# Kernel optimization log

Measured on AMD Instinct MI355X. Metric: run time of the kernel, lower is better.

Reference implementation:

```python
import jax, jax.numpy as jnp
import numpy as np

EARLY_IT = 32                      # prefix K-columns used for the statistical test
TEST_STAT_BOUND = -2.053748910631823  # scipy.stats.norm.ppf(0.02)
EPS = 1e-12
STATS_W = 1.0                      # scalar stats affine (stats_affine_mode='scalar')
STATS_B = 0.0


def setup_inputs() -> dict:
    key = jax.random.key(0)
    k1, k2, k3 = jax.random.split(key, 3)
    M, K, N = 4096, 4096, 16384    # tokens, in_features, out_features (OPT-6.7B fc1)
    x = jax.random.normal(k1, (M, K), dtype=jnp.float32)
    weight = jax.random.normal(k2, (N, K), dtype=jnp.float32) * 0.02
    bias = jax.random.normal(k3, (N,), dtype=jnp.float32) * 0.02
    return {"x": x, "weight": weight, "bias": bias}


def reference(x, weight, bias):
    # x: [M, K], weight: [N, K], bias: [N]
    E = EARLY_IT
    inv_n = jnp.float32(1.0 / E)

    xe = x[:, :E]                                  # [M, E]
    we = weight[:, :E]                             # [N, E]
    # Partial matmul over the first E reduction columns + elementwise-squared matmul
    y1 = jnp.einsum('mk,nk->mn', xe, we)           # [M, N]
    cum_sq = jnp.einsum('mk,nk->mn', xe * xe, we * we)  # [M, N]

    # Statistical early-termination test (z-test-like)
    cur_mean = y1 * inv_n * STATS_W + STATS_B
    cur_var = (cum_sq * inv_n - cur_mean * cur_mean) * (STATS_W * STATS_W)
    denom = jnp.sqrt(jnp.maximum(cur_var * inv_n, EPS))
    test_stats = cur_mean / denom
    passed = test_stats < TEST_STAT_BOUND          # [M, N] bool: True -> skip, output 0

    # Tail GEMM over remaining K-E columns
    y_tail = jnp.einsum('mk,nk->mn', x[:, E:], weight[:, E:])
    y = y1 + y_tail + bias[None, :]
    return jnp.where(passed, jnp.float32(0.0), y)
```

## Files before the change

### kernel.cpp

```cpp
#include <hip/hip_runtime.h>
#include <cstdint>
#include <cmath>

#define MDIM 4096
#define KDIM 4096
#define NDIM 16384
#define TEST_BOUND -2.053748910631823

typedef unsigned short u16;
typedef __attribute__((ext_vector_type(8))) short short8;
typedef __attribute__((ext_vector_type(4))) float floatx4;

__device__ __forceinline__ u16 f2bf(float f) {
  union { float f; uint32_t u; } c; c.f = f;
  uint32_t r = c.u + 0x7fffu + ((c.u >> 16) & 1u);
  return (u16)(r >> 16);
}

__global__ __launch_bounds__(256) void cvt_kernel(const float4* __restrict__ in,
                                                  ushort4* __restrict__ out, int n4) {
  int stride = gridDim.x * 256;
  for (int i = blockIdx.x * 256 + threadIdx.x; i < n4; i += stride) {
    float4 v = in[i];
    ushort4 o;
    o.x = f2bf(v.x); o.y = f2bf(v.y); o.z = f2bf(v.z); o.w = f2bf(v.w);
    out[i] = o;
  }
}

__global__ __launch_bounds__(256) void stats_kernel(const float* __restrict__ x,
                                                    const float* __restrict__ w,
                                                    unsigned char* __restrict__ mask) {
  __shared__ float Xs[64][33];
  __shared__ float Ws[64][33];
  const int bn = blockIdx.x;
  const int bm = blockIdx.y;
  const int t = threadIdx.x;
  for (int e = t; e < 64 * 32; e += 256) {
    int r = e >> 5, c = e & 31;
    Xs[r][c] = x[(size_t)(bm * 64 + r) * KDIM + c];
    Ws[r][c] = w[(size_t)(bn * 64 + r) * KDIM + c];
  }
  __syncthreads();
  const int tn = (t & 15) * 4;
  const int tm = (t >> 4) * 4;
  float y1[4][4] = {}, q[4][4] = {};
  for (int k = 0; k < 32; ++k) {
    float xv[4], wv[4], xx[4], ww[4];
#pragma unroll
    for (int i = 0; i < 4; ++i) { xv[i] = Xs[tm + i][k]; xx[i] = __fmul_rn(xv[i], xv[i]); }
#pragma unroll
    for (int j = 0; j < 4; ++j) { wv[j] = Ws[tn + j][k]; ww[j] = __fmul_rn(wv[j], wv[j]); }
#pragma unroll
    for (int i = 0; i < 4; ++i)
#pragma unroll
      for (int j = 0; j < 4; ++j) {
        y1[i][j] = __fadd_rn(y1[i][j], __fmul_rn(xv[i], wv[j]));
        q[i][j]  = __fadd_rn(q[i][j],  __fmul_rn(xx[i], ww[j]));
      }
  }
#pragma unroll
  for (int i = 0; i < 4; ++i)
#pragma unroll
    for (int j = 0; j < 4; ++j) {
      float mean = __fmul_rn(y1[i][j], 0.03125f);
      float var  = __fsub_rn(__fmul_rn(q[i][j], 0.03125f), __fmul_rn(mean, mean));
      float varn = __fmul_rn(var, 0.03125f);
      float den  = __fsqrt_rn(fmaxf(varn, 1e-12f));
      float ts   = __fdiv_rn(mean, den);
      bool passed = ts < (float)TEST_BOUND;
      mask[(size_t)(bm * 64 + tm + i) * NDIM + (bn * 64 + tn + j)] = passed ? 1u : 0u;
    }
}

#define BM 256
#define BN 256
#define BK 64

typedef const __attribute__((address_space(1))) uint32_t* as1_u32p;
typedef __attribute__((address_space(3))) uint32_t* as3_u32p;

__device__ __forceinline__ void async_ld16(const void* g, void* l) {
  __builtin_amdgcn_global_load_lds((as1_u32p)g, (as3_u32p)l, 16, 0, 0);
}

__device__ __forceinline__ void stage_half(const u16* __restrict__ src, size_t grow0,
                                           int k0, u16* lds, int tid) {
  const int r = tid >> 3;
  const int c = (((tid & 7) ^ (r & 7)) << 3);
  const u16* g0 = src + (grow0 + (size_t)r) * KDIM + (size_t)(k0 + c);
  u16* l0 = lds + (size_t)(tid & ~63) * 8;
  async_ld16(g0, l0);
  async_ld16(g0 + (size_t)64 * KDIM, l0 + 4096);
}

__global__ __launch_bounds__(512, 2) void gemm_kernel(const u16* __restrict__ A,
                                                      const u16* __restrict__ B,
                                                      const float* __restrict__ bias,
                                                      const unsigned char* __restrict__ mask,
                                                      float* __restrict__ C) {
  __shared__ __align__(16) u16 As[2][BM * BK];
  __shared__ __align__(16) u16 Bs[2][BN * BK];

  const int bid = blockIdx.x;
  const int swz = (bid & 7) * ((MDIM / BM) * (NDIM / BN) / 8) + (bid >> 3);
  const int bm = swz & 15;
  const int bn = swz >> 4;

  const int tid = threadIdx.x;
  const int w = tid >> 6, l = tid & 63;
  const int lm = l & 15, quad = l >> 4;
  const int wm_i = w >> 2;
  const int wn_i = w & 3;
  const int sw8 = (lm & 7) << 3;
  const int c0 = (quad * 8) ^ sw8;
  const int c1 = (32 + quad * 8) ^ sw8;

  const size_t abase = (size_t)bm * BM;
  const size_t bbase = (size_t)bn * BN;

  floatx4 acc[8][4];
#pragma unroll
  for (int i = 0; i < 8; ++i)
#pragma unroll
    for (int j = 0; j < 4; ++j) acc[i][j] = (floatx4){0.f, 0.f, 0.f, 0.f};

  stage_half(A, abase,       0,  &As[0][0],    tid);
  stage_half(B, bbase,       0,  &Bs[0][0],    tid);
  stage_half(B, bbase + 128, 0,  &Bs[0][8192], tid);
  stage_half(A, abase + 128, 0,  &As[0][8192], tid);
  asm volatile("s_waitcnt vmcnt(4)" ::: "memory");
  stage_half(A, abase,       BK, &As[1][0],    tid);
  stage_half(B, bbase,       BK, &Bs[1][0],    tid);
  stage_half(B, bbase + 128, BK, &Bs[1][8192], tid);
  asm volatile("s_waitcnt vmcnt(6)" ::: "memory");
  __builtin_amdgcn_s_barrier();

  short8 a[4][2], b[4][2];

  for (int kt = 0; kt < KDIM / BK; ++kt) {
    u16* Ab = &As[kt & 1][0];
    u16* Bb = &Bs[kt & 1][0];
    const int kn1 = (kt + 1 <= 63 ? kt + 1 : 63) * BK;
    const int kn2 = (kt + 2 <= 63 ? kt + 2 : 63) * BK;

#pragma unroll
    for (int i4 = 0; i4 < 4; ++i4) {
      const int row = wm_i * 16 + i4 * 32 + lm;
      a[i4][0] = *(const short8*)&Ab[row * 64 + c0];
      a[i4][1] = *(const short8*)&Ab[row * 64 + c1];
    }
#pragma unroll
    for (int j = 0; j < 2; ++j) {
      const int row = wn_i * 16 + j * 64 + lm;
      b[j][0] = *(const short8*)&Bb[row * 64 + c0];
      b[j][1] = *(const short8*)&Bb[row * 64 + c1];
    }
    stage_half(A, abase + 128, kn1, &As[(kt + 1) & 1][8192], tid);
    __builtin_amdgcn_s_barrier();
    asm volatile("s_waitcnt lgkmcnt(0)" ::: "memory");
    __builtin_amdgcn_sched_barrier(0);
    __builtin_amdgcn_s_setprio(1);
#pragma unroll
    for (int i4 = 0; i4 < 4; ++i4)
#pragma unroll
      for (int j = 0; j < 2; ++j) {
        acc[i4][j] = __builtin_amdgcn_mfma_f32_16x16x32_bf16(a[i4][0], b[j][0], acc[i4][j], 0, 0, 0);
        acc[i4][j] = __builtin_amdgcn_mfma_f32_16x16x32_bf16(a[i4][1], b[j][1], acc[i4][j], 0, 0, 0);
      }
    __builtin_amdgcn_s_setprio(0);
    __builtin_amdgcn_s_barrier();

#pragma unroll
    for (int j = 2; j < 4; ++j) {
      const int row = wn_i * 16 + j * 64 + lm;
      b[j][0] = *(const short8*)&Bb[row * 64 + c0];
      b[j][1] = *(const short8*)&Bb[row * 64 + c1];
    }
    stage_half(A, abase, kn2, &As[kt & 1][0], tid);
    __builtin_amdgcn_s_barrier();
    asm volatile("s_waitcnt lgkmcnt(0)" ::: "memory");
    __builtin_amdgcn_sched_barrier(0);
    __builtin_amdgcn_s_setprio(1);
#pragma unroll
    for (int i4 = 0; i4 < 4; ++i4)
#pragma unroll
      for (int j = 2; j < 4; ++j) {
        acc[i4][j] = __builtin_amdgcn_mfma_f32_16x16x32_bf16(a[i4][0], b[j][0], acc[i4][j], 0, 0, 0);
        acc[i4][j] = __builtin_amdgcn_mfma_f32_16x16x32_bf16(a[i4][1], b[j][1], acc[i4][j], 0, 0, 0);
      }
    __builtin_amdgcn_s_setprio(0);
    __builtin_amdgcn_s_barrier();

#pragma unroll
    for (int i4 = 0; i4 < 4; ++i4) {
      const int row = wm_i * 16 + (4 + i4) * 32 + lm;
      a[i4][0] = *(const short8*)&Ab[row * 64 + c0];
      a[i4][1] = *(const short8*)&Ab[row * 64 + c1];
    }
    stage_half(B, bbase, kn2, &Bs[kt & 1][0], tid);
    __builtin_amdgcn_s_barrier();
    asm volatile("s_waitcnt lgkmcnt(0)" ::: "memory");
    __builtin_amdgcn_sched_barrier(0);
    __builtin_amdgcn_s_setprio(1);
#pragma unroll
    for (int i4 = 0; i4 < 4; ++i4)
#pragma unroll
      for (int j = 0; j < 2; ++j) {
        acc[4 + i4][j] = __builtin_amdgcn_mfma_f32_16x16x32_bf16(a[i4][0], b[j][0], acc[4 + i4][j], 0, 0, 0);
        acc[4 + i4][j] = __builtin_amdgcn_mfma_f32_16x16x32_bf16(a[i4][1], b[j][1], acc[4 + i4][j], 0, 0, 0);
      }
    __builtin_amdgcn_s_setprio(0);
    __builtin_amdgcn_s_barrier();

    stage_half(B, bbase + 128, kn2, &Bs[kt & 1][8192], tid);
    __builtin_amdgcn_s_barrier();
    __builtin_amdgcn_s_setprio(1);
#pragma unroll
    for (int i4 = 0; i4 < 4; ++i4)
#pragma unroll
      for (int j = 2; j < 4; ++j) {
        acc[4 + i4][j] = __builtin_amdgcn_mfma_f32_16x16x32_bf16(a[i4][0], b[j][0], acc[4 + i4][j], 0, 0, 0);
        acc[4 + i4][j] = __builtin_amdgcn_mfma_f32_16x16x32_bf16(a[i4][1], b[j][1], acc[4 + i4][j], 0, 0, 0);
      }
    __builtin_amdgcn_s_setprio(0);
    asm volatile("s_waitcnt vmcnt(6)" ::: "memory");
    __builtin_amdgcn_s_barrier();
  }

  float bv[4];
#pragma unroll
  for (int j = 0; j < 4; ++j) bv[j] = bias[bbase + wn_i * 16 + j * 64 + lm];
#pragma unroll
  for (int i = 0; i < 8; ++i) {
    const int mrow = wm_i * 16 + i * 32 + quad * 4;
#pragma unroll
    for (int r = 0; r < 4; ++r) {
      const size_t gm = abase + (size_t)(mrow + r);
      const size_t rowoff = gm * NDIM + bbase;
#pragma unroll
      for (int j = 0; j < 4; ++j) {
        const size_t off = rowoff + (size_t)(wn_i * 16 + j * 64 + lm);
        float y = acc[i][j][r] + bv[j];
        C[off] = mask[off] ? 0.0f : y;
      }
    }
  }
}

extern "C" void kernel_launch(void* const* d_in, const int* in_sizes, int n_in,
                              void* d_out, int out_size, void* d_ws, size_t ws_size,
                              hipStream_t stream) {
  const float* x = (const float*)d_in[0];
  const float* w = (const float*)d_in[1];
  const float* bias = (const float*)d_in[2];
  float* out = (float*)d_out;

  u16* xbf = (u16*)d_ws;
  u16* wbf = xbf + (size_t)MDIM * KDIM;
  unsigned char* mask = (unsigned char*)(wbf + (size_t)NDIM * KDIM);

  cvt_kernel<<<2048, 256, 0, stream>>>((const float4*)x, (ushort4*)xbf, MDIM * KDIM / 4);
  cvt_kernel<<<8192, 256, 0, stream>>>((const float4*)w, (ushort4*)wbf, NDIM * KDIM / 4);
  stats_kernel<<<dim3(NDIM / 64, MDIM / 64), 256, 0, stream>>>(x, w, mask);
  gemm_kernel<<<(MDIM / BM) * (NDIM / BN), 512, 0, stream>>>(xbf, wbf, bias, mask, out);
}
```

Measured before the change: 1.195 ms.

## Switch GEMM inner loop to 32x32x16 bf16 MFMA tiles

Replaces the 16x16x32 MFMA tiling with 32x32x16 MFMA instructions. Each wave now holds 4x2 floatx16 accumulators instead of 8x4 floatx4. Fewer, larger MFMAs need less LDS fragment traffic per FLOP, and a partial lgkmcnt wait lets the first MFMAs start before all fragment loads land. The prefetch k-index clamps at the last tile were removed, so the final iterations may read past K into adjacent rows of the workspace. The epilogue store indexing was rewritten for the 32x32 output layout.

```diff
diff --git a/kernel.cpp b/kernel.cpp
--- a/kernel.cpp
+++ b/kernel.cpp
@@ -9,7 +9,7 @@
 
 typedef unsigned short u16;
 typedef __attribute__((ext_vector_type(8))) short short8;
-typedef __attribute__((ext_vector_type(4))) float floatx4;
+typedef __attribute__((ext_vector_type(16))) float floatx16;
 
 __device__ __forceinline__ u16 f2bf(float f) {
   union { float f; uint32_t u; } c; c.f = f;
@@ -103,27 +103,34 @@
   __shared__ __align__(16) u16 Bs[2][BN * BK];
 
   const int bid = blockIdx.x;
-  const int swz = (bid & 7) * ((MDIM / BM) * (NDIM / BN) / 8) + (bid >> 3);
+  const int swz = (bid & 7) * 128 + (bid >> 3);
   const int bm = swz & 15;
   const int bn = swz >> 4;
 
   const int tid = threadIdx.x;
   const int w = tid >> 6, l = tid & 63;
-  const int lm = l & 15, quad = l >> 4;
+  const int ln = l & 31;
+  const int kh = (l >> 5) << 3;
   const int wm_i = w >> 2;
   const int wn_i = w & 3;
-  const int sw8 = (lm & 7) << 3;
-  const int c0 = (quad * 8) ^ sw8;
-  const int c1 = (32 + quad * 8) ^ sw8;
+  const int swx = (ln & 7) << 3;
+
+  int ck[4];
+#pragma unroll
+  for (int ks = 0; ks < 4; ++ks) ck[ks] = (ks * 16 + kh) ^ swx;
+  const int arow = (wm_i * 32 + ln) * 64;
+  const int brow = (wn_i * 32 + ln) * 64;
 
   const size_t abase = (size_t)bm * BM;
   const size_t bbase = (size_t)bn * BN;
 
-  floatx4 acc[8][4];
-#pragma unroll
-  for (int i = 0; i < 8; ++i)
-#pragma unroll
-    for (int j = 0; j < 4; ++j) acc[i][j] = (floatx4){0.f, 0.f, 0.f, 0.f};
+  floatx16 acc[4][2];
+#pragma unroll
+  for (int i = 0; i < 4; ++i)
+#pragma unroll
+    for (int j = 0; j < 2; ++j)
+#pragma unroll
+      for (int r = 0; r < 16; ++r) acc[i][j][r] = 0.f;
 
   stage_half(A, abase,       0,  &As[0][0],    tid);
   stage_half(B, bbase,       0,  &Bs[0][0],    tid);
@@ -136,111 +143,98 @@
   asm volatile("s_waitcnt vmcnt(6)" ::: "memory");
   __builtin_amdgcn_s_barrier();
 
-  short8 a[4][2], b[4][2];
+  short8 a[2][4], b[2][4];
 
   for (int kt = 0; kt < KDIM / BK; ++kt) {
     u16* Ab = &As[kt & 1][0];
     u16* Bb = &Bs[kt & 1][0];
-    const int kn1 = (kt + 1 <= 63 ? kt + 1 : 63) * BK;
-    const int kn2 = (kt + 2 <= 63 ? kt + 2 : 63) * BK;
-
-#pragma unroll
-    for (int i4 = 0; i4 < 4; ++i4) {
-      const int row = wm_i * 16 + i4 * 32 + lm;
-      a[i4][0] = *(const short8*)&Ab[row * 64 + c0];
-      a[i4][1] = *(const short8*)&Ab[row * 64 + c1];
-    }
+    const int kn1 = (kt + 1) * BK;
+    const int kn2 = (kt + 2) * BK;
+
+#pragma unroll
+    for (int s = 0; s < 2; ++s)
+#pragma unroll
+      for (int ks = 0; ks < 4; ++ks)
+        a[s][ks] = *(const short8*)&Ab[arow + s * 4096 + ck[ks]];
+#pragma unroll
+    for (int ks = 0; ks < 4; ++ks) b[0][ks] = *(const short8*)&Bb[brow + ck[ks]];
+#pragma unroll
+    for (int ks = 0; ks < 4; ++ks) b[1][ks] = *(const short8*)&Bb[brow + 8192 + ck[ks]];
+    stage_half(A, abase + 128, kn1, &As[(kt + 1) & 1][8192], tid);
+    __builtin_amdgcn_s_barrier();
+    asm volatile("s_waitcnt lgkmcnt(4)" ::: "memory");
+    __builtin_amdgcn_sched_barrier(0);
+    __builtin_amdgcn_s_setprio(1);
+#pragma unroll
+    for (int ks = 0; ks < 4; ++ks)
+#pragma unroll
+      for (int s = 0; s < 2; ++s)
+        acc[s][0] = __builtin_amdgcn_mfma_f32_32x32x16_bf16(a[s][ks], b[0][ks], acc[s][0], 0, 0, 0);
+    __builtin_amdgcn_s_setprio(0);
+    __builtin_amdgcn_sched_barrier(0);
+    __builtin_amdgcn_s_barrier();
+
+    stage_half(A, abase, kn2, &As[kt & 1][0], tid);
+    __builtin_amdgcn_s_barrier();
+    asm volatile("s_waitcnt lgkmcnt(0)" ::: "memory");
+    __builtin_amdgcn_sched_barrier(0);
+    __builtin_amdgcn_s_setprio(1);
+#pragma unroll
+    for (int ks = 0; ks < 4; ++ks)
+#pragma unroll
+      for (int s = 0; s < 2; ++s)
+        acc[s][1] = __builtin_amdgcn_mfma_f32_32x32x16_bf16(a[s][ks], b[1][ks], acc[s][1], 0, 0, 0);
+    __builtin_amdgcn_s_setprio(0);
+    __builtin_amdgcn_sched_barrier(0);
+    __builtin_amdgcn_s_barrier();
+
+#pragma unroll
+    for (int s = 0; s < 2; ++s)
+#pragma unroll
+      for (int ks = 0; ks < 4; ++ks)
+        a[s][ks] = *(const short8*)&Ab[8192 + arow + s * 4096 + ck[ks]];
+    stage_half(B, bbase, kn2, &Bs[kt & 1][0], tid);
+    __builtin_amdgcn_s_barrier();
+    asm volatile("s_waitcnt lgkmcnt(0)" ::: "memory");
+    __builtin_amdgcn_sched_barrier(0);
+    __builtin_amdgcn_s_setprio(1);
+#pragma unroll
+    for (int ks = 0; ks < 4; ++ks)
+#pragma unroll
+      for (int s = 0; s < 2; ++s)
+        acc[2 + s][0] = __builtin_amdgcn_mfma_f32_32x32x16_bf16(a[s][ks], b[0][ks], acc[2 + s][0], 0, 0, 0);
+    __builtin_amdgcn_s_setprio(0);
+    __builtin_amdgcn_sched_barrier(0);
+    __builtin_amdgcn_s_barrier();
+
+    stage_half(B, bbase + 128, kn2, &Bs[kt & 1][8192], tid);
+    __builtin_amdgcn_s_barrier();
+    __builtin_amdgcn_s_setprio(1);
+#pragma unroll
+    for (int ks = 0; ks < 4; ++ks)
+#pragma unroll
+      for (int s = 0; s < 2; ++s)
+        acc[2 + s][1] = __builtin_amdgcn_mfma_f32_32x32x16_bf16(a[s][ks], b[1][ks], acc[2 + s][1], 0, 0, 0);
+    __builtin_amdgcn_s_setprio(0);
+    asm volatile("s_waitcnt vmcnt(6)" ::: "memory");
+    __builtin_amdgcn_sched_barrier(0);
+    __builtin_amdgcn_s_barrier();
+  }
+
+  float bv[2];
+#pragma unroll
+  for (int j = 0; j < 2; ++j) bv[j] = bias[bbase + wn_i * 32 + j * 128 + ln];
+  const int rbase = (l >> 5) * 4;
+#pragma unroll
+  for (int i = 0; i < 4; ++i) {
+    const size_t growf = abase + (size_t)(wm_i * 32 + i * 64);
 #pragma unroll
     for (int j = 0; j < 2; ++j) {
-      const int row = wn_i * 16 + j * 64 + lm;
-      b[j][0] = *(const short8*)&Bb[row * 64 + c0];
-      b[j][1] = *(const short8*)&Bb[row * 64 + c1];
-    }
-    stage_half(A, abase + 128, kn1, &As[(kt + 1) & 1][8192], tid);
-    __builtin_amdgcn_s_barrier();
-    asm volatile("s_waitcnt lgkmcnt(0)" ::: "memory");
-    __builtin_amdgcn_sched_barrier(0);
-    __builtin_amdgcn_s_setprio(1);
-#pragma unroll
-    for (int i4 = 0; i4 < 4; ++i4)
-#pragma unroll
-      for (int j = 0; j < 2; ++j) {
-        acc[i4][j] = __builtin_amdgcn_mfma_f32_16x16x32_bf16(a[i4][0], b[j][0], acc[i4][j], 0, 0, 0);
-        acc[i4][j] = __builtin_amdgcn_mfma_f32_16x16x32_bf16(a[i4][1], b[j][1], acc[i4][j], 0, 0, 0);
-      }
-    __builtin_amdgcn_s_setprio(0);
-    __builtin_amdgcn_s_barrier();
-
-#pragma unroll
-    for (int j = 2; j < 4; ++j) {
-      const int row = wn_i * 16 + j * 64 + lm;
-      b[j][0] = *(const short8*)&Bb[row * 64 + c0];
-      b[j][1] = *(const short8*)&Bb[row * 64 + c1];
-    }
-    stage_half(A, abase, kn2, &As[kt & 1][0], tid);
-    __builtin_amdgcn_s_barrier();
-    asm volatile("s_waitcnt lgkmcnt(0)" ::: "memory");
-    __builtin_amdgcn_sched_barrier(0);
-    __builtin_amdgcn_s_setprio(1);
-#pragma unroll
-    for (int i4 = 0; i4 < 4; ++i4)
-#pragma unroll
-      for (int j = 2; j < 4; ++j) {
-        acc[i4][j] = __builtin_amdgcn_mfma_f32_16x16x32_bf16(a[i4][0], b[j][0], acc[i4][j], 0, 0, 0);
-        acc[i4][j] = __builtin_amdgcn_mfma_f32_16x16x32_bf16(a[i4][1], b[j][1], acc[i4][j], 0, 0, 0);
-      }
-    __builtin_amdgcn_s_setprio(0);
-    __builtin_amdgcn_s_barrier();
-
-#pragma unroll
-    for (int i4 = 0; i4 < 4; ++i4) {
-      const int row = wm_i * 16 + (4 + i4) * 32 + lm;
-      a[i4][0] = *(const short8*)&Ab[row * 64 + c0];
-      a[i4][1] = *(const short8*)&Ab[row * 64 + c1];
-    }
-    stage_half(B, bbase, kn2, &Bs[kt & 1][0], tid);
-    __builtin_amdgcn_s_barrier();
-    asm volatile("s_waitcnt lgkmcnt(0)" ::: "memory");
-    __builtin_amdgcn_sched_barrier(0);
-    __builtin_amdgcn_s_setprio(1);
-#pragma unroll
-    for (int i4 = 0; i4 < 4; ++i4)
-#pragma unroll
-      for (int j = 0; j < 2; ++j) {
-        acc[4 + i4][j] = __builtin_amdgcn_mfma_f32_16x16x32_bf16(a[i4][0], b[j][0], acc[4 + i4][j], 0, 0, 0);
-        acc[4 + i4][j] = __builtin_amdgcn_mfma_f32_16x16x32_bf16(a[i4][1], b[j][1], acc[4 + i4][j], 0, 0, 0);
-      }
-    __builtin_amdgcn_s_setprio(0);
-    __builtin_amdgcn_s_barrier();
-
-    stage_half(B, bbase + 128, kn2, &Bs[kt & 1][8192], tid);
-    __builtin_amdgcn_s_barrier();
-    __builtin_amdgcn_s_setprio(1);
-#pragma unroll
-    for (int i4 = 0; i4 < 4; ++i4)
-#pragma unroll
-      for (int j = 2; j < 4; ++j) {
-        acc[4 + i4][j] = __builtin_amdgcn_mfma_f32_16x16x32_bf16(a[i4][0], b[j][0], acc[4 + i4][j], 0, 0, 0);
-        acc[4 + i4][j] = __builtin_amdgcn_mfma_f32_16x16x32_bf16(a[i4][1], b[j][1], acc[4 + i4][j], 0, 0, 0);
-      }
-    __builtin_amdgcn_s_setprio(0);
-    asm volatile("s_waitcnt vmcnt(6)" ::: "memory");
-    __builtin_amdgcn_s_barrier();
-  }
-
-  float bv[4];
-#pragma unroll
-  for (int j = 0; j < 4; ++j) bv[j] = bias[bbase + wn_i * 16 + j * 64 + lm];
-#pragma unroll
-  for (int i = 0; i < 8; ++i) {
-    const int mrow = wm_i * 16 + i * 32 + quad * 4;
-#pragma unroll
-    for (int r = 0; r < 4; ++r) {
-      const size_t gm = abase + (size_t)(mrow + r);
-      const size_t rowoff = gm * NDIM + bbase;
-#pragma unroll
-      for (int j = 0; j < 4; ++j) {
-        const size_t off = rowoff + (size_t)(wn_i * 16 + j * 64 + lm);
+      const size_t coloff = bbase + (size_t)(wn_i * 32 + j * 128 + ln);
+#pragma unroll
+      for (int r = 0; r < 16; ++r) {
+        const int mloc = (r & 3) + 8 * (r >> 2) + rbase;
+        const size_t off = (growf + mloc) * NDIM + coloff;
         float y = acc[i][j][r] + bv[j];
         C[off] = mask[off] ? 0.0f : y;
       }
```

New measurement: 1.213 ms. No clear change (+1.5%).
